# Performance work log

Hardware: AMD Instinct MI355X
Metric: run time of the kernel (lower is better)

Reference implementation:

```python
import jax, jax.numpy as jnp
import numpy as np

N_NODES = 50000
N_EDGES = 800000
D_IN = 96
D_HID = 96
N_CLASSES = 10
NUM_GRAPHS = 64


def setup_inputs() -> dict:
    key = jax.random.key(0)
    ks = jax.random.split(key, 6)
    x = jax.random.normal(ks[0], (N_NODES, D_IN), dtype=jnp.float32)
    edge_index = jax.random.randint(ks[1], (2, N_EDGES), 0, N_NODES, dtype=jnp.int64)
    batch = jnp.sort(jax.random.randint(ks[2], (N_NODES,), 0, NUM_GRAPHS, dtype=jnp.int64))
    s1 = 1.0 / np.sqrt(D_IN)
    s2 = 1.0 / np.sqrt(D_HID)
    W1 = jax.random.normal(ks[3], (D_IN, D_HID), dtype=jnp.float32) * s1
    b1 = jnp.zeros((D_HID,), dtype=jnp.float32)
    W2 = jax.random.normal(ks[4], (D_HID, D_HID), dtype=jnp.float32) * s2
    b2 = jnp.zeros((D_HID,), dtype=jnp.float32)
    Wfc = jax.random.normal(ks[5], (D_HID, N_CLASSES), dtype=jnp.float32) * s2
    bfc = jnp.zeros((N_CLASSES,), dtype=jnp.float32)
    return {"x": x, "edge_index": edge_index, "batch": batch,
            "W1": W1, "b1": b1, "W2": W2, "b2": b2, "Wfc": Wfc, "bfc": bfc}


def _gcn_conv(x, src, dst, W, b, n_nodes):
    """PyG GCNConv: add self-loops, sym-normalize, scatter-add, + bias.
    Self-loop term folded in analytically as h_i * d_i^2."""
    h = x @ W  # [N, D]
    ones = jnp.ones_like(src, dtype=h.dtype)
    deg = jax.ops.segment_sum(ones, dst, num_segments=n_nodes) + 1.0  # +1 self-loop
    dinv = jax.lax.rsqrt(deg)  # deg >= 1, always finite
    norm = dinv[src] * dinv[dst]  # [E]
    msg = h[src] * norm[:, None]  # [E, D]
    agg = jax.ops.segment_sum(msg, dst, num_segments=n_nodes)
    return agg + h * (dinv * dinv)[:, None] + b


def reference(x, edge_index, batch, W1, b1, W2, b2, Wfc, bfc):
    src, dst = edge_index[0], edge_index[1]
    n = x.shape[0]
    h = jax.nn.relu(_gcn_conv(x, src, dst, W1, b1, n))
    h = jax.nn.relu(_gcn_conv(h, src, dst, W2, b2, n))
    # global_mean_pool over graph ids
    sums = jax.ops.segment_sum(h, batch, num_segments=NUM_GRAPHS)  # [G, D]
    cnts = jax.ops.segment_sum(jnp.ones((n,), h.dtype), batch, num_segments=NUM_GRAPHS)
    pooled = sums / jnp.maximum(cnts, 1.0)[:, None]
    return pooled @ Wfc + bfc
```

## Files before the change

kernel.cpp:

```cpp
#include <hip/hip_runtime.h>
#include <hip/hip_fp16.h>
#include <type_traits>

#define N_NODES 50000
#define N_EDGES 800000
#define D 96
#define NGRAPH 64
#define NCLS 10
#define GEMM_BLOCKS 521
#define SLOT_LOG 6
#define SLOT_STRIDE 64
#define GATHER_BLOCKS 3125
#define EPB 1024
#define FILL_CHUNKS ((N_EDGES + EPB - 1) / EPB)
#define NODES_PER_PART 6250

struct h4v { __half2 lo, hi; };

__global__ __launch_bounds__(256) void slot_fill(const int* __restrict__ src,
                                                 const int* __restrict__ dst,
                                                 int* __restrict__ degCnt,
                                                 unsigned short* __restrict__ slot) {
    int blk = blockIdx.x;
    int part = blk & 7;
    int base = (blk >> 3) * EPB + threadIdx.x;
#pragma unroll
    for (int k = 0; k < EPB / 256; ++k) {
        int e = base + k * 256;
        if (e < N_EDGES) {
            int d0 = dst[e];
            if (d0 / NODES_PER_PART == part) {
                int pos = atomicAdd(&degCnt[d0], 1);
                slot[((size_t)d0 << SLOT_LOG) + (pos & (SLOT_STRIDE - 1))] =
                    (unsigned short)src[e];
            }
        }
    }
}

__global__ __launch_bounds__(256) void dinv_bounds(const int* __restrict__ degCnt,
                                                   float* __restrict__ dinv,
                                                   const int* __restrict__ batch,
                                                   int* __restrict__ start) {
    int i = blockIdx.x * 256 + threadIdx.x;
    if (i >= N_NODES) return;
    dinv[i] = rsqrtf((float)degCnt[i] + 1.0f);
    int bb = batch[i];
    if (i == 0) {
        for (int g = 0; g <= bb; ++g) start[g] = 0;
    } else {
        int p = batch[i - 1];
        for (int g = p + 1; g <= bb; ++g) start[g] = i;
    }
    if (i == N_NODES - 1) {
        for (int g = bb + 1; g <= NGRAPH; ++g) start[g] = N_NODES;
    }
}

template <typename T>
__global__ __launch_bounds__(384) void gemm96(const T* __restrict__ X,
                                              const float* __restrict__ W,
                                              const float* __restrict__ dinv,
                                              __half* __restrict__ Yh) {
    __shared__ __align__(16) float Xl[96 * 100];
    __shared__ __align__(16) float Wl[96 * 96];
    int tid = threadIdx.x;
    int rowBase = blockIdx.x * 96;

#pragma unroll
    for (int i = 0; i < 6; ++i) {
        int f4 = tid + i * 384;
        int r = f4 / 24, c = f4 - r * 24;
        int gr = rowBase + r;
        float4 v;
        if (gr < N_NODES) {
            if constexpr (std::is_same<T, float>::value) {
                v = ((const float4*)X)[(size_t)gr * 24 + c];
            } else {
                h4v hv = ((const h4v*)X)[(size_t)gr * 24 + c];
                float2 a = __half22float2(hv.lo), b = __half22float2(hv.hi);
                v = make_float4(a.x, a.y, b.x, b.y);
            }
        } else {
            v = make_float4(0.f, 0.f, 0.f, 0.f);
        }
        *(float4*)&Xl[r * 100 + c * 4] = v;
    }
    const float4* W4 = (const float4*)W;
#pragma unroll
    for (int i = 0; i < 6; ++i) {
        int f4 = tid + i * 384;
        ((float4*)Wl)[f4] = W4[f4];
    }
    __syncthreads();

    int c4 = tid % 24;
    int r0 = tid / 24;
    float4 acc[6];
#pragma unroll
    for (int j = 0; j < 6; ++j) acc[j] = make_float4(0.f, 0.f, 0.f, 0.f);

    for (int k0 = 0; k0 < 96; k0 += 4) {
        float4 wv0 = *(const float4*)&Wl[(k0 + 0) * 96 + c4 * 4];
        float4 wv1 = *(const float4*)&Wl[(k0 + 1) * 96 + c4 * 4];
        float4 wv2 = *(const float4*)&Wl[(k0 + 2) * 96 + c4 * 4];
        float4 wv3 = *(const float4*)&Wl[(k0 + 3) * 96 + c4 * 4];
#pragma unroll
        for (int j = 0; j < 6; ++j) {
            float4 xj = *(const float4*)&Xl[(r0 + 16 * j) * 100 + k0];
            acc[j].x = fmaf(xj.x, wv0.x, acc[j].x);
            acc[j].y = fmaf(xj.x, wv0.y, acc[j].y);
            acc[j].z = fmaf(xj.x, wv0.z, acc[j].z);
            acc[j].w = fmaf(xj.x, wv0.w, acc[j].w);
            acc[j].x = fmaf(xj.y, wv1.x, acc[j].x);
            acc[j].y = fmaf(xj.y, wv1.y, acc[j].y);
            acc[j].z = fmaf(xj.y, wv1.z, acc[j].z);
            acc[j].w = fmaf(xj.y, wv1.w, acc[j].w);
            acc[j].x = fmaf(xj.z, wv2.x, acc[j].x);
            acc[j].y = fmaf(xj.z, wv2.y, acc[j].y);
            acc[j].z = fmaf(xj.z, wv2.z, acc[j].z);
            acc[j].w = fmaf(xj.z, wv2.w, acc[j].w);
            acc[j].x = fmaf(xj.w, wv3.x, acc[j].x);
            acc[j].y = fmaf(xj.w, wv3.y, acc[j].y);
            acc[j].z = fmaf(xj.w, wv3.z, acc[j].z);
            acc[j].w = fmaf(xj.w, wv3.w, acc[j].w);
        }
    }

#pragma unroll
    for (int j = 0; j < 6; ++j) {
        int gr = rowBase + r0 + 16 * j;
        if (gr < N_NODES) {
            float sc = dinv[gr];
            __half2 h0 = __float22half2_rn(make_float2(acc[j].x * sc, acc[j].y * sc));
            __half2 h1 = __float22half2_rn(make_float2(acc[j].z * sc, acc[j].w * sc));
            __half2* dsth = (__half2*)&Yh[(size_t)gr * 96 + c4 * 4];
            dsth[0] = h0;
            dsth[1] = h1;
        }
    }
}

__device__ __forceinline__ float4 gcr_row(const __half* __restrict__ hh,
                                          const int* __restrict__ degCnt,
                                          const unsigned short* __restrict__ slot,
                                          const float* __restrict__ dinv,
                                          const float* __restrict__ bias,
                                          int i, int q) {
    int dg = degCnt[i];
    if (dg > SLOT_STRIDE) dg = SLOT_STRIDE;
    const unsigned short* sl = slot + ((size_t)i << SLOT_LOG);

    h4v sv = *(const h4v*)&hh[(size_t)i * 96 + q * 4];
    float2 sa = __half22float2(sv.lo), sb = __half22float2(sv.hi);
    float4 acc = make_float4(sa.x, sa.y, sb.x, sb.y);

    int j = 0;
    while (j + 8 <= dg) {
        int u[8];
#pragma unroll
        for (int m = 0; m < 8; ++m) u[m] = sl[j + m];
        h4v v[8];
#pragma unroll
        for (int m = 0; m < 8; ++m)
            v[m] = *(const h4v*)&hh[(size_t)u[m] * 96 + q * 4];
#pragma unroll
        for (int m = 0; m < 8; ++m) {
            float2 fa = __half22float2(v[m].lo);
            float2 fb = __half22float2(v[m].hi);
            acc.x += fa.x; acc.y += fa.y; acc.z += fb.x; acc.w += fb.y;
        }
        j += 8;
    }
    if (j + 4 <= dg) {
        int u[4];
#pragma unroll
        for (int m = 0; m < 4; ++m) u[m] = sl[j + m];
        h4v v[4];
#pragma unroll
        for (int m = 0; m < 4; ++m)
            v[m] = *(const h4v*)&hh[(size_t)u[m] * 96 + q * 4];
#pragma unroll
        for (int m = 0; m < 4; ++m) {
            float2 fa = __half22float2(v[m].lo);
            float2 fb = __half22float2(v[m].hi);
            acc.x += fa.x; acc.y += fa.y; acc.z += fb.x; acc.w += fb.y;
        }
        j += 4;
    }
    for (; j < dg; ++j) {
        int u = sl[j];
        h4v v = *(const h4v*)&hh[(size_t)u * 96 + q * 4];
        float2 fa = __half22float2(v.lo);
        float2 fb = __half22float2(v.hi);
        acc.x += fa.x; acc.y += fa.y; acc.z += fb.x; acc.w += fb.y;
    }

    float di = dinv[i];
    float4 bv = ((const float4*)bias)[q];
    float4 v;
    v.x = fmaxf(fmaf(acc.x, di, bv.x), 0.f);
    v.y = fmaxf(fmaf(acc.y, di, bv.y), 0.f);
    v.z = fmaxf(fmaf(acc.z, di, bv.z), 0.f);
    v.w = fmaxf(fmaf(acc.w, di, bv.w), 0.f);
    return v;
}

__global__ __launch_bounds__(384) void gather_combine_relu(
        const __half* __restrict__ hh,
        const int* __restrict__ degCnt,
        const unsigned short* __restrict__ slot,
        const float* __restrict__ dinv,
        const float* __restrict__ bias,
        __half* __restrict__ out) {
    int tid = blockIdx.x * 384 + threadIdx.x;
    int i = tid / 24;
    int q = tid - i * 24;
    float4 v = gcr_row(hh, degCnt, slot, dinv, bias, i, q);
    h4v o;
    o.lo = __float22half2_rn(make_float2(v.x, v.y));
    o.hi = __float22half2_rn(make_float2(v.z, v.w));
    ((h4v*)out)[tid] = o;
}

__global__ __launch_bounds__(384) void gather_pool(
        const __half* __restrict__ hh,
        const int* __restrict__ degCnt,
        const unsigned short* __restrict__ slot,
        const float* __restrict__ dinv,
        const float* __restrict__ bias,
        const int* __restrict__ batch,
        float* __restrict__ blkpart) {
    __shared__ float4 red[384];
    __shared__ int flg[16];
    int blk = blockIdx.x;
    int tid = threadIdx.x;
    int base = blk * 16;
    int i = base + tid / 24;
    int q = tid % 24;

    float4 v = gcr_row(hh, degCnt, slot, dinv, bias, i, q);
    red[tid] = v;
    int g0 = batch[base];
    if (q == 0) flg[tid / 24] = (batch[i] != g0) ? 1 : 0;
    __syncthreads();

    if (tid < 48) {
        int b = tid / 24, q2 = tid % 24;
        float4 s = make_float4(0.f, 0.f, 0.f, 0.f);
        for (int n = 0; n < 16; ++n) {
            if (flg[n] == b) {
                float4 r = red[n * 24 + q2];
                s.x += r.x; s.y += r.y; s.z += r.z; s.w += r.w;
            }
        }
        *(float4*)&blkpart[((size_t)blk * 2 + b) * 96 + q2 * 4] = s;
    }
}

__global__ __launch_bounds__(96) void pool_final(const float* __restrict__ blkpart,
                                                 const int* __restrict__ start,
                                                 const int* __restrict__ batch,
                                                 const float* __restrict__ Wfc,
                                                 const float* __restrict__ bfc,
                                                 float* __restrict__ out) {
    __shared__ float pl[D];
    int g = blockIdx.x;
    int t = threadIdx.x;
    int s = start[g], e = start[g + 1];
    float v = 0.f;
    if (e > s) {
        int bs = s >> 4, be = (e - 1) >> 4;
        for (int blk = bs; blk <= be; ++blk) {
            int g0 = batch[blk << 4];
            int bucket = (g0 == g) ? 0 : 1;
            v += blkpart[((size_t)blk * 2 + bucket) * 96 + t];
        }
    }
    float n = (float)(e - s);
    pl[t] = v / fmaxf(n, 1.0f);
    __syncthreads();
    if (t < NCLS) {
        float acc = bfc[t];
#pragma unroll
        for (int k = 0; k < D; ++k)
            acc = fmaf(pl[k], Wfc[k * NCLS + t], acc);
        out[g * NCLS + t] = acc;
    }
}

extern "C" void kernel_launch(void* const* d_in, const int* in_sizes, int n_in,
                              void* d_out, int out_size, void* d_ws, size_t ws_size,
                              hipStream_t stream) {
    const float* x   = (const float*)d_in[0];
    const int*   ei  = (const int*)d_in[1];
    const int*   bat = (const int*)d_in[2];
    const float* W1  = (const float*)d_in[3];
    const float* b1  = (const float*)d_in[4];
    const float* W2  = (const float*)d_in[5];
    const float* b2  = (const float*)d_in[6];
    const float* Wfc = (const float*)d_in[7];
    const float* bfc = (const float*)d_in[8];
    float* out = (float*)d_out;

    const int* srcp = ei;
    const int* dstp = ei + N_EDGES;

    float* dinv    = (float*)d_ws;
    __half* B      = (__half*)(dinv + 50048);
    __half* Ph     = B + (size_t)N_NODES * D;
    float* blkpart = (float*)(Ph + (size_t)N_NODES * D);
    int*   start   = (int*)(blkpart + (size_t)GATHER_BLOCKS * 2 * D);
    int*   degCnt  = start + 72;
    unsigned short* slot = (unsigned short*)(degCnt + N_NODES);

    hipMemsetAsync(degCnt, 0, N_NODES * sizeof(int), stream);
    slot_fill<<<FILL_CHUNKS * 8, 256, 0, stream>>>(srcp, dstp, degCnt, slot);
    dinv_bounds<<<(N_NODES + 255) / 256, 256, 0, stream>>>(degCnt, dinv, bat, start);

    gemm96<float><<<GEMM_BLOCKS, 384, 0, stream>>>(x, W1, dinv, Ph);
    gather_combine_relu<<<GATHER_BLOCKS, 384, 0, stream>>>(Ph, degCnt, slot, dinv, b1, B);

    gemm96<__half><<<GEMM_BLOCKS, 384, 0, stream>>>(B, W2, dinv, Ph);
    gather_pool<<<GATHER_BLOCKS, 384, 0, stream>>>(Ph, degCnt, slot, dinv, b2, bat, blkpart);

    pool_final<<<NGRAPH, 96, 0, stream>>>(blkpart, start, bat, Wfc, bfc, out);
}
```

Baseline: 265.9 us.

## Fuse layer-1 neighbor gather and ReLU into the layer-2 GEMM tile load

The layer-1 aggregation (gather, normalize, bias, ReLU) is computed directly while filling the shared-memory X tile of the second GEMM, instead of running as a separate kernel. This removes the intermediate half-precision activation buffer write and read and one kernel launch. In exchange, the gather runs with far fewer blocks and sequential per-thread work under a large shared-memory footprint, which may reduce latency hiding for the irregular loads.

```diff
diff --git a/kernel.cpp b/kernel.cpp
--- a/kernel.cpp
+++ b/kernel.cpp
@@ -1,6 +1,5 @@
 #include <hip/hip_runtime.h>
 #include <hip/hip_fp16.h>
-#include <type_traits>
 
 #define N_NODES 50000
 #define N_EDGES 800000
@@ -57,8 +56,72 @@
     }
 }
 
-template <typename T>
-__global__ __launch_bounds__(384) void gemm96(const T* __restrict__ X,
+__device__ __forceinline__ float4 gcr_row(const __half* __restrict__ hh,
+                                          const int* __restrict__ degCnt,
+                                          const unsigned short* __restrict__ slot,
+                                          const float* __restrict__ dinv,
+                                          const float* __restrict__ bias,
+                                          int i, int q) {
+    int dg = degCnt[i];
+    if (dg > SLOT_STRIDE) dg = SLOT_STRIDE;
+    const unsigned short* sl = slot + ((size_t)i << SLOT_LOG);
+
+    h4v sv = *(const h4v*)&hh[(size_t)i * 96 + q * 4];
+    float2 sa = __half22float2(sv.lo), sb = __half22float2(sv.hi);
+    float4 acc = make_float4(sa.x, sa.y, sb.x, sb.y);
+
+    int j = 0;
+    while (j + 8 <= dg) {
+        int u[8];
+#pragma unroll
+        for (int m = 0; m < 8; ++m) u[m] = sl[j + m];
+        h4v v[8];
+#pragma unroll
+        for (int m = 0; m < 8; ++m)
+            v[m] = *(const h4v*)&hh[(size_t)u[m] * 96 + q * 4];
+#pragma unroll
+        for (int m = 0; m < 8; ++m) {
+            float2 fa = __half22float2(v[m].lo);
+            float2 fb = __half22float2(v[m].hi);
+            acc.x += fa.x; acc.y += fa.y; acc.z += fb.x; acc.w += fb.y;
+        }
+        j += 8;
+    }
+    if (j + 4 <= dg) {
+        int u[4];
+#pragma unroll
+        for (int m = 0; m < 4; ++m) u[m] = sl[j + m];
+        h4v v[4];
+#pragma unroll
+        for (int m = 0; m < 4; ++m)
+            v[m] = *(const h4v*)&hh[(size_t)u[m] * 96 + q * 4];
+#pragma unroll
+        for (int m = 0; m < 4; ++m) {
+            float2 fa = __half22float2(v[m].lo);
+            float2 fb = __half22float2(v[m].hi);
+            acc.x += fa.x; acc.y += fa.y; acc.z += fb.x; acc.w += fb.y;
+        }
+        j += 4;
+    }
+    for (; j < dg; ++j) {
+        int u = sl[j];
+        h4v v = *(const h4v*)&hh[(size_t)u * 96 + q * 4];
+        float2 fa = __half22float2(v.lo);
+        float2 fb = __half22float2(v.hi);
+        acc.x += fa.x; acc.y += fa.y; acc.z += fb.x; acc.w += fb.y;
+    }
+
+    float di = dinv[i];
+    float4 bv = ((const float4*)bias)[q];
+    float4 v;
+    v.x = fmaxf(fmaf(acc.x, di, bv.x), 0.f);
+    v.y = fmaxf(fmaf(acc.y, di, bv.y), 0.f);
+    v.z = fmaxf(fmaf(acc.z, di, bv.z), 0.f);
+    v.w = fmaxf(fmaf(acc.w, di, bv.w), 0.f);
+    return v;
+}
+
+__global__ __launch_bounds__(384) void gemm96(const float* __restrict__ X,
                                               const float* __restrict__ W,
                                               const float* __restrict__ dinv,
                                               __half* __restrict__ Yh) {
@@ -67,23 +130,14 @@
     int tid = threadIdx.x;
     int rowBase = blockIdx.x * 96;
 
+    const float4* X4 = (const float4*)X;
 #pragma unroll
     for (int i = 0; i < 6; ++i) {
         int f4 = tid + i * 384;
         int r = f4 / 24, c = f4 - r * 24;
         int gr = rowBase + r;
-        float4 v;
-        if (gr < N_NODES) {
-            if constexpr (std::is_same<T, float>::value) {
-                v = ((const float4*)X)[(size_t)gr * 24 + c];
-            } else {
-                h4v hv = ((const h4v*)X)[(size_t)gr * 24 + c];
-                float2 a = __half22float2(hv.lo), b = __half22float2(hv.hi);
-                v = make_float4(a.x, a.y, b.x, b.y);
-            }
-        } else {
-            v = make_float4(0.f, 0.f, 0.f, 0.f);
-        }
+        float4 v = (gr < N_NODES) ? X4[(size_t)gr * 24 + c]
+                                  : make_float4(0.f, 0.f, 0.f, 0.f);
         *(float4*)&Xl[r * 100 + c * 4] = v;
     }
     const float4* W4 = (const float4*)W;
@@ -141,86 +195,83 @@
     }
 }
 
-__device__ __forceinline__ float4 gcr_row(const __half* __restrict__ hh,
-                                          const int* __restrict__ degCnt,
-                                          const unsigned short* __restrict__ slot,
-                                          const float* __restrict__ dinv,
-                                          const float* __restrict__ bias,
-                                          int i, int q) {
-    int dg = degCnt[i];
-    if (dg > SLOT_STRIDE) dg = SLOT_STRIDE;
-    const unsigned short* sl = slot + ((size_t)i << SLOT_LOG);
-
-    h4v sv = *(const h4v*)&hh[(size_t)i * 96 + q * 4];
-    float2 sa = __half22float2(sv.lo), sb = __half22float2(sv.hi);
-    float4 acc = make_float4(sa.x, sa.y, sb.x, sb.y);
-
-    int j = 0;
-    while (j + 8 <= dg) {
-        int u[8];
-#pragma unroll
-        for (int m = 0; m < 8; ++m) u[m] = sl[j + m];
-        h4v v[8];
-#pragma unroll
-        for (int m = 0; m < 8; ++m)
-            v[m] = *(const h4v*)&hh[(size_t)u[m] * 96 + q * 4];
-#pragma unroll
-        for (int m = 0; m < 8; ++m) {
-            float2 fa = __half22float2(v[m].lo);
-            float2 fb = __half22float2(v[m].hi);
-            acc.x += fa.x; acc.y += fa.y; acc.z += fb.x; acc.w += fb.y;
-        }
-        j += 8;
-    }
-    if (j + 4 <= dg) {
-        int u[4];
-#pragma unroll
-        for (int m = 0; m < 4; ++m) u[m] = sl[j + m];
-        h4v v[4];
-#pragma unroll
-        for (int m = 0; m < 4; ++m)
-            v[m] = *(const h4v*)&hh[(size_t)u[m] * 96 + q * 4];
-#pragma unroll
-        for (int m = 0; m < 4; ++m) {
-            float2 fa = __half22float2(v[m].lo);
-            float2 fb = __half22float2(v[m].hi);
-            acc.x += fa.x; acc.y += fa.y; acc.z += fb.x; acc.w += fb.y;
-        }
-        j += 4;
-    }
-    for (; j < dg; ++j) {
-        int u = sl[j];
-        h4v v = *(const h4v*)&hh[(size_t)u * 96 + q * 4];
-        float2 fa = __half22float2(v.lo);
-        float2 fb = __half22float2(v.hi);
-        acc.x += fa.x; acc.y += fa.y; acc.z += fb.x; acc.w += fb.y;
-    }
-
-    float di = dinv[i];
-    float4 bv = ((const float4*)bias)[q];
-    float4 v;
-    v.x = fmaxf(fmaf(acc.x, di, bv.x), 0.f);
-    v.y = fmaxf(fmaf(acc.y, di, bv.y), 0.f);
-    v.z = fmaxf(fmaf(acc.z, di, bv.z), 0.f);
-    v.w = fmaxf(fmaf(acc.w, di, bv.w), 0.f);
-    return v;
-}
-
-__global__ __launch_bounds__(384) void gather_combine_relu(
-        const __half* __restrict__ hh,
+__global__ __launch_bounds__(384) void gather_gemm(
+        const __half* __restrict__ Ph1,
         const int* __restrict__ degCnt,
         const unsigned short* __restrict__ slot,
         const float* __restrict__ dinv,
-        const float* __restrict__ bias,
-        __half* __restrict__ out) {
-    int tid = blockIdx.x * 384 + threadIdx.x;
-    int i = tid / 24;
-    int q = tid - i * 24;
-    float4 v = gcr_row(hh, degCnt, slot, dinv, bias, i, q);
-    h4v o;
-    o.lo = __float22half2_rn(make_float2(v.x, v.y));
-    o.hi = __float22half2_rn(make_float2(v.z, v.w));
-    ((h4v*)out)[tid] = o;
+        const float* __restrict__ b1,
+        const float* __restrict__ W2,
+        __half* __restrict__ Ph2) {
+    __shared__ __align__(16) float Xl[96 * 100];
+    __shared__ __align__(16) float Wl[96 * 96];
+    int tid = threadIdx.x;
+    int rowBase = blockIdx.x * 96;
+
+    const float4* W4 = (const float4*)W2;
+#pragma unroll
+    for (int i = 0; i < 6; ++i) {
+        int f4 = tid + i * 384;
+        ((float4*)Wl)[f4] = W4[f4];
+    }
+
+#pragma unroll
+    for (int i = 0; i < 6; ++i) {
+        int p = tid + i * 384;
+        int r = p / 24, c = p - (p / 24) * 24;
+        int gr = rowBase + r;
+        float4 v = (gr < N_NODES)
+                       ? gcr_row(Ph1, degCnt, slot, dinv, b1, gr, c)
+                       : make_float4(0.f, 0.f, 0.f, 0.f);
+        *(float4*)&Xl[r * 100 + c * 4] = v;
+    }
+    __syncthreads();
+
+    int c4 = tid % 24;
+    int r0 = tid / 24;
+    float4 acc[6];
+#pragma unroll
+    for (int j = 0; j < 6; ++j) acc[j] = make_float4(0.f, 0.f, 0.f, 0.f);
+
+    for (int k0 = 0; k0 < 96; k0 += 4) {
+        float4 wv0 = *(const float4*)&Wl[(k0 + 0) * 96 + c4 * 4];
+        float4 wv1 = *(const float4*)&Wl[(k0 + 1) * 96 + c4 * 4];
+        float4 wv2 = *(const float4*)&Wl[(k0 + 2) * 96 + c4 * 4];
+        float4 wv3 = *(const float4*)&Wl[(k0 + 3) * 96 + c4 * 4];
+#pragma unroll
+        for (int j = 0; j < 6; ++j) {
+            float4 xj = *(const float4*)&Xl[(r0 + 16 * j) * 100 + k0];
+            acc[j].x = fmaf(xj.x, wv0.x, acc[j].x);
+            acc[j].y = fmaf(xj.x, wv0.y, acc[j].y);
+            acc[j].z = fmaf(xj.x, wv0.z, acc[j].z);
+            acc[j].w = fmaf(xj.x, wv0.w, acc[j].w);
+            acc[j].x = fmaf(xj.y, wv1.x, acc[j].x);
+            acc[j].y = fmaf(xj.y, wv1.y, acc[j].y);
+            acc[j].z = fmaf(xj.y, wv1.z, acc[j].z);
+            acc[j].w = fmaf(xj.y, wv1.w, acc[j].w);
+            acc[j].x = fmaf(xj.z, wv2.x, acc[j].x);
+            acc[j].y = fmaf(xj.z, wv2.y, acc[j].y);
+            acc[j].z = fmaf(xj.z, wv2.z, acc[j].z);
+            acc[j].w = fmaf(xj.z, wv2.w, acc[j].w);
+            acc[j].x = fmaf(xj.w, wv3.x, acc[j].x);
+            acc[j].y = fmaf(xj.w, wv3.y, acc[j].y);
+            acc[j].z = fmaf(xj.w, wv3.z, acc[j].z);
+            acc[j].w = fmaf(xj.w, wv3.w, acc[j].w);
+        }
+    }
+
+#pragma unroll
+    for (int j = 0; j < 6; ++j) {
+        int gr = rowBase + r0 + 16 * j;
+        if (gr < N_NODES) {
+            float sc = dinv[gr];
+            __half2 h0 = __float22half2_rn(make_float2(acc[j].x * sc, acc[j].y * sc));
+            __half2 h1 = __float22half2_rn(make_float2(acc[j].z * sc, acc[j].w * sc));
+            __half2* dsth = (__half2*)&Ph2[(size_t)gr * 96 + c4 * 4];
+            dsth[0] = h0;
+            dsth[1] = h1;
+        }
+    }
 }
 
 __global__ __launch_bounds__(384) void gather_pool(
@@ -307,9 +358,9 @@
     const int* dstp = ei + N_EDGES;
 
     float* dinv    = (float*)d_ws;
-    __half* B      = (__half*)(dinv + 50048);
-    __half* Ph     = B + (size_t)N_NODES * D;
-    float* blkpart = (float*)(Ph + (size_t)N_NODES * D);
+    __half* Ph1    = (__half*)(dinv + 50048);
+    __half* Ph2    = Ph1 + (size_t)N_NODES * D;
+    float* blkpart = (float*)(Ph2 + (size_t)N_NODES * D);
     int*   start   = (int*)(blkpart + (size_t)GATHER_BLOCKS * 2 * D);
     int*   degCnt  = start + 72;
     unsigned short* slot = (unsigned short*)(degCnt + N_NODES);
@@ -318,11 +369,11 @@
     slot_fill<<<FILL_CHUNKS * 8, 256, 0, stream>>>(srcp, dstp, degCnt, slot);
     dinv_bounds<<<(N_NODES + 255) / 256, 256, 0, stream>>>(degCnt, dinv, bat, start);
 
-    gemm96<float><<<GEMM_BLOCKS, 384, 0, stream>>>(x, W1, dinv, Ph);
-    gather_combine_relu<<<GATHER_BLOCKS, 384, 0, stream>>>(Ph, degCnt, slot, dinv, b1, B);
-
-    gemm96<__half><<<GEMM_BLOCKS, 384, 0, stream>>>(B, W2, dinv, Ph);
-    gather_pool<<<GATHER_BLOCKS, 384, 0, stream>>>(Ph, degCnt, slot, dinv, b2, bat, blkpart);
+    gemm96<<<GEMM_BLOCKS, 384, 0, stream>>>(x, W1, dinv, Ph1);
+
+    gather_gemm<<<GEMM_BLOCKS, 384, 0, stream>>>(Ph1, degCnt, slot, dinv, b1, W2, Ph2);
+
+    gather_pool<<<GATHER_BLOCKS, 384, 0, stream>>>(Ph2, degCnt, slot, dinv, b2, bat, blkpart);
 
     pool_final<<<NGRAPH, 96, 0, stream>>>(blkpart, start, bat, Wfc, bfc, out);
 }
```

Result: slower. 307.1 us (+15.5%).
